# Performance work log

Hardware: AMD Instinct MI355X
Metric: run time of the kernel (lower is better)

## Reference

```python
import jax, jax.numpy as jnp
import numpy as np

B, T, C, H = 4, 2048, 1024, 16
D = C // H  # head dim = 64

def precompute_rope(dim, max_pos):
    # rope_cache[t, i] = (cos(t*theta_i), sin(t*theta_i)), theta_i = 10000^(-2i/dim)
    i = jnp.arange(dim // 2, dtype=jnp.float32)
    theta = 1.0 / (10000.0 ** (2.0 * i / dim))
    t = jnp.arange(max_pos, dtype=jnp.float32)[:, None]
    ang = t * theta[None, :]
    return jnp.stack([jnp.cos(ang), jnp.sin(ang)], axis=-1)  # (max_pos, dim/2, 2)

def apply_rope(x, rope):
    # x: (B, H, T, D); complex multiply rope * x over pairs of channels
    Tq = x.shape[2]
    xr = x.reshape(x.shape[0], x.shape[1], Tq, D // 2, 2)
    a, b = xr[..., 0], xr[..., 1]
    c = rope[:Tq, :, 0]  # (T, D/2)
    s = rope[:Tq, :, 1]
    real = a * c - b * s
    imag = a * s + b * c
    return jnp.stack([real, imag], axis=-1).reshape(x.shape)

def setup_inputs() -> dict:
    key = jax.random.key(0)
    ks = jax.random.split(key, 9)
    scale = 1.0 / np.sqrt(C)
    def w(k):
        return jax.random.uniform(k, (C, C), jnp.float32, -scale, scale)
    def bvec(k):
        return jax.random.uniform(k, (C,), jnp.float32, -scale, scale)
    return {
        "x": jax.random.normal(ks[0], (B, T, C), jnp.float32),
        "Wq": w(ks[1]), "bq": bvec(ks[2]),
        "Wk": w(ks[3]), "bk": bvec(ks[4]),
        "Wv": w(ks[5]), "bv": bvec(ks[6]),
        "Wp": w(ks[7]), "bp": bvec(ks[8]),
        "rope_cache": precompute_rope(D, T),
    }

def reference(x, Wq, bq, Wk, bk, Wv, bv, Wp, bp, rope_cache):
    B_, T_, C_ = x.shape
    def heads(y):
        return y.reshape(B_, T_, H, D).transpose(0, 2, 1, 3)  # (B,H,T,D)
    q = heads(x @ Wq.T + bq)
    k = heads(x @ Wk.T + bk)
    v = heads(x @ Wv.T + bv)
    q = apply_rope(q, rope_cache)
    k = apply_rope(k, rope_cache)
    att = jnp.einsum("bhqd,bhkd->bhqk", q, k) * (1.0 / np.sqrt(D))
    causal = jnp.tril(jnp.ones((T_, T_), dtype=bool))
    att = jnp.where(causal, att, jnp.float32(-1e10))
    att = jax.nn.softmax(att, axis=-1)
    y = jnp.einsum("bhqk,bhkd->bhqd", att, v)
    y = y.transpose(0, 2, 1, 3).reshape(B_, T_, C_)
    return y @ Wp.T + bp
```

## Files before the change

kernel.cpp:

```cpp
#include <hip/hip_runtime.h>

#define DEVINL __device__ __forceinline__

typedef unsigned short u16;
typedef __attribute__((ext_vector_type(4))) short s16x4;
typedef __attribute__((ext_vector_type(8))) short s16x8;
typedef __attribute__((ext_vector_type(4))) float f32x4;

static constexpr int Bb = 4, Tt = 2048, Cc = 1024, Hh = 16, Dd = 64;
static constexpr int Mm = Bb * Tt;
static constexpr int KK = Cc;

DEVINL float bf2f(u16 u) { return __uint_as_float(((unsigned)u) << 16); }
DEVINL u16 f2bf(float f) {
  unsigned b = __float_as_uint(f);
  b += 0x7fff + ((b >> 16) & 1);
  return (u16)(b >> 16);
}
DEVINL unsigned cvtpk(float lo, float hi) {
  unsigned r;
  asm("v_cvt_pk_bf16_f32 %0, %1, %2" : "=v"(r) : "v"(lo), "v"(hi));
  return r;
}

#define GLDS(gsrc, ldst) \
  __builtin_amdgcn_global_load_lds((const __attribute__((address_space(1))) void*)(gsrc), \
                                   (__attribute__((address_space(3))) void*)(ldst), 16, 0, 0)

__global__ void cvt_bf16(const float* __restrict__ src, u16* __restrict__ dst, int n4) {
  int i = blockIdx.x * blockDim.x + threadIdx.x;
  int st = gridDim.x * blockDim.x;
  for (int g = i; g < n4; g += st) {
    float4 v = ((const float4*)src)[g];
    uint2 o;
    o.x = (unsigned)f2bf(v.x) | ((unsigned)f2bf(v.y) << 16);
    o.y = (unsigned)f2bf(v.z) | ((unsigned)f2bf(v.w) << 16);
    ((uint2*)dst)[g] = o;
  }
}

struct Cvt4Args { const float* s[4]; u16* d[4]; };
__global__ void cvt4(Cvt4Args a, int n4) {
  const float* __restrict__ src = a.s[blockIdx.y];
  u16* __restrict__ dst = a.d[blockIdx.y];
  int i = blockIdx.x * blockDim.x + threadIdx.x;
  int st = gridDim.x * blockDim.x;
  for (int g = i; g < n4; g += st) {
    float4 v = ((const float4*)src)[g];
    uint2 o;
    o.x = (unsigned)f2bf(v.x) | ((unsigned)f2bf(v.y) << 16);
    o.y = (unsigned)f2bf(v.z) | ((unsigned)f2bf(v.w) << 16);
    ((uint2*)dst)[g] = o;
  }
}

__global__ void rope_kernel(u16* __restrict__ q, u16* __restrict__ k,
                            const float* __restrict__ cache) {
  const float CS = 0.18033688f;
  const int total = Bb * Hh * Tt * 8;
  int i = blockIdx.x * blockDim.x + threadIdx.x;
  int st = gridDim.x * blockDim.x;
  for (int g = i; g < total; g += st) {
    int off = g * 8;
    int t = (off >> 6) & (Tt - 1);
    int d0 = off & 63;
    const float* cp = cache + t * 64 + d0;
    float4 c0 = *(const float4*)cp;
    float4 c1 = *(const float4*)(cp + 4);
    float cs[8] = {c0.x, c0.y, c0.z, c0.w, c1.x, c1.y, c1.z, c1.w};
    s16x8 qv = *(s16x8*)(q + off);
    s16x8 kv = *(s16x8*)(k + off);
    s16x8 qo, ko;
#pragma unroll
    for (int p = 0; p < 4; ++p) {
      float c = cs[2 * p], s = cs[2 * p + 1];
      float a = bf2f((u16)qv[2 * p]), b = bf2f((u16)qv[2 * p + 1]);
      qo[2 * p] = (short)f2bf((a * c - b * s) * CS);
      qo[2 * p + 1] = (short)f2bf((a * s + b * c) * CS);
      a = bf2f((u16)kv[2 * p]); b = bf2f((u16)kv[2 * p + 1]);
      ko[2 * p] = (short)f2bf(a * c - b * s);
      ko[2 * p + 1] = (short)f2bf(a * s + b * c);
    }
    *(s16x8*)(q + off) = qo;
    *(s16x8*)(k + off) = ko;
  }
}

#define GEMM_PROLOG()                                              \
  const int tid = threadIdx.x, w = tid >> 6, l = tid & 63;         \
  const int lr = l & 15, lg = l >> 4;                              \
  const int m0 = blockIdx.x * 128, n0 = blockIdx.y * 128;          \
  const int wr = w >> 1, wc = w & 1;                               \
  f32x4 zero = {0.f, 0.f, 0.f, 0.f};                               \
  f32x4 acc[4][4];                                                 \
  _Pragma("unroll") for (int i = 0; i < 4; ++i)                    \
      _Pragma("unroll") for (int j = 0; j < 4; ++j) acc[i][j] = zero; \
  const int srow = l >> 3;                                         \
  const int scolsw = ((l & 7) ^ (l >> 3)) * 8;

#define GEMM_KLOOP(Aptr, Wptr)                                                         \
  for (int k0 = 0; k0 < KK; k0 += 64) {                                                \
    _Pragma("unroll") for (int i = 0; i < 4; ++i) {                                    \
      int row = i * 32 + w * 8 + srow;                                                 \
      GLDS(Aptr + (size_t)(m0 + row) * KK + k0 + scolsw, &As[(i * 32 + w * 8) * 64]);  \
      GLDS(Wptr + (size_t)(n0 + row) * KK + k0 + scolsw, &Bs[(i * 32 + w * 8) * 64]);  \
    }                                                                                  \
    __syncthreads();                                                                   \
    _Pragma("unroll") for (int kk = 0; kk < 2; ++kk) {                                 \
      s16x8 af[4], bfr[4];                                                             \
      _Pragma("unroll") for (int i = 0; i < 4; ++i)                                    \
          af[i] = *(const s16x8*)&As[(wr * 64 + i * 16 + lr) * 64 +                    \
                                     ((kk * 32 + lg * 8) ^ ((lr & 7) << 3))];          \
      _Pragma("unroll") for (int j = 0; j < 4; ++j)                                    \
          bfr[j] = *(const s16x8*)&Bs[(wc * 64 + j * 16 + lr) * 64 +                   \
                                      ((kk * 32 + lg * 8) ^ ((lr & 7) << 3))];         \
      _Pragma("unroll") for (int i = 0; i < 4; ++i)                                    \
          _Pragma("unroll") for (int j = 0; j < 4; ++j)                                \
              acc[i][j] =                                                              \
                  __builtin_amdgcn_mfma_f32_16x16x32_bf16(af[i], bfr[j], acc[i][j], 0, 0, 0); \
    }                                                                                  \
    __syncthreads();                                                                   \
  }

__global__ __launch_bounds__(256) void gemm_qk(const u16* __restrict__ A,
                                               const u16* __restrict__ W0,
                                               const u16* __restrict__ W1,
                                               const float* __restrict__ b0,
                                               const float* __restrict__ b1,
                                               u16* __restrict__ O0, u16* __restrict__ O1) {
  __shared__ __align__(16) u16 As[128 * 64];
  __shared__ __align__(16) u16 Bs[128 * 64];
  const int z = blockIdx.z;
  const u16* __restrict__ Wt = z ? W1 : W0;
  const float* __restrict__ bias = z ? b1 : b0;
  u16* __restrict__ O = z ? O1 : O0;
  GEMM_PROLOG()
  GEMM_KLOOP(A, Wt)
#pragma unroll
  for (int j = 0; j < 4; ++j) {
    int ncol = n0 + wc * 64 + j * 16 + lr;
    float bj = bias[ncol];
    int hh = ncol >> 6, dd = ncol & 63;
#pragma unroll
    for (int i = 0; i < 4; ++i) {
#pragma unroll
      for (int r = 0; r < 4; ++r) {
        int mrow = m0 + wr * 64 + i * 16 + lg * 4 + r;
        int bb2 = mrow >> 11, tt2 = mrow & (Tt - 1);
        O[(((size_t)bb2 * Hh + hh) * Tt + tt2) * Dd + dd] = f2bf(acc[i][j][r] + bj);
      }
    }
  }
}

__global__ __launch_bounds__(256) void gemm_v(const u16* __restrict__ A,
                                              const u16* __restrict__ Wt,
                                              const float* __restrict__ bias,
                                              u16* __restrict__ O) {
  __shared__ __align__(16) u16 As[128 * 64];
  __shared__ __align__(16) u16 Bs[128 * 64];
  __shared__ __align__(16) u16 Ts[128 * 64];
  GEMM_PROLOG()
  GEMM_KLOOP(A, Wt)
  const int bb2 = m0 >> 11, tloc = m0 & (Tt - 1);
#pragma unroll
  for (int p = 0; p < 2; ++p) {
    if (p) __syncthreads();
    if (wr == p) {
#pragma unroll
      for (int j = 0; j < 4; ++j) {
        int ncl = wc * 64 + j * 16 + lr;
        float bj = bias[n0 + ncl];
        int xw = (ncl & 3) << 2;
#pragma unroll
        for (int i = 0; i < 4; ++i) {
          s16x4 pk;
#pragma unroll
          for (int r = 0; r < 4; ++r) pk[r] = (short)f2bf(acc[i][j][r] + bj);
          *(s16x4*)&Ts[ncl * 64 + (((i * 4 + lg) ^ xw) << 2)] = pk;
        }
      }
    }
    __syncthreads();
    const int rn = tid >> 3, t8 = tid & 7;
#pragma unroll
    for (int it = 0; it < 4; ++it) {
      int rown = it * 32 + rn;
      int slot = (t8 * 2) ^ ((rown & 3) << 2);
      s16x8 v = *(const s16x8*)&Ts[rown * 64 + slot * 4];
      int ncol = n0 + rown;
      int hh2 = ncol >> 6, dd = ncol & 63;
      *(s16x8*)&O[(((size_t)bb2 * Hh + hh2) * Dd + dd) * Tt + tloc + p * 64 + t8 * 8] = v;
    }
  }
}

__global__ __launch_bounds__(256) void gemm_proj(const u16* __restrict__ A,
                                                 const u16* __restrict__ Wt,
                                                 const float* __restrict__ bias,
                                                 float* __restrict__ O) {
  __shared__ __align__(16) u16 As[128 * 64];
  __shared__ __align__(16) u16 Bs[128 * 64];
  GEMM_PROLOG()
  GEMM_KLOOP(A, Wt)
#pragma unroll
  for (int j = 0; j < 4; ++j) {
    int ncol = n0 + wc * 64 + j * 16 + lr;
    float bj = bias[ncol];
#pragma unroll
    for (int i = 0; i < 4; ++i) {
#pragma unroll
      for (int r = 0; r < 4; ++r) {
        int mrow = m0 + wr * 64 + i * 16 + lg * 4 + r;
        O[(size_t)mrow * Cc + ncol] = acc[i][j][r] + bj;
      }
    }
  }
}

__global__ __launch_bounds__(256, 4) void attn_kernel(const u16* __restrict__ Q,
                                                      const u16* __restrict__ K,
                                                      const u16* __restrict__ VTg,
                                                      u16* __restrict__ Out) {
  __shared__ __align__(16) u16 Ks[2][64 * 64];
  __shared__ __align__(16) u16 VTs[2][64 * 64];
  __shared__ __align__(16) u16 Ps[4 * 16 * 32];
  const int tid = threadIdx.x, w = tid >> 6, l = tid & 63;
  const int lr = l & 15, lg = l >> 4;
  const int n = blockIdx.x + 16 * blockIdx.y;
  const int bh = ((n & 7) << 3) + (n >> 7);
  const int qpair = (n >> 3) & 15;
  const size_t base = (size_t)bh * Tt * Dd;
  const u16* Qp = Q + base;
  const u16* Kp = K + base;
  const u16* Vp = VTg + base;
  const int bb2 = bh >> 4, hh = bh & 15;
  const float NEG = -3.0e9f;
  f32x4 zero = {0.f, 0.f, 0.f, 0.f};
  const int krow_l = l >> 3, kc8sw = ((l & 7) ^ (l >> 3)) * 8;
  const int psw = (lr >> 1) & 3;

  auto process = [&](int qt) {
    const int qb0 = qt * 64;
    const int qrow = qb0 + w * 16 + lr;
    const int qg = qrow;
    s16x8 qf[2];
    qf[0] = *(const s16x8*)(Qp + (size_t)qrow * 64 + lg * 8);
    qf[1] = *(const s16x8*)(Qp + (size_t)qrow * 64 + 32 + lg * 8);
    f32x4 o[4] = {zero, zero, zero, zero};
    float m = -3e38f, lsum = 0.f;
    const int ktiles = qt + 1;
    auto stage = [&](int kt, int buf) {
      const int kk0 = kt * 64;
#pragma unroll
      for (int i = 0; i < 2; ++i) {
        int row = i * 32 + w * 8 + krow_l;
        GLDS(Kp + (size_t)(kk0 + row) * 64 + kc8sw, &Ks[buf][(i * 32 + w * 8) * 64]);
        GLDS(Vp + (size_t)row * Tt + kk0 + kc8sw, &VTs[buf][(i * 32 + w * 8) * 64]);
      }
    };
    stage(0, 0);
    for (int kt = 0; kt < ktiles; ++kt) {
      const int buf = kt & 1;
      if (kt + 1 < ktiles) {
        stage(kt + 1, buf ^ 1);
        asm volatile("s_waitcnt vmcnt(4)" ::: "memory");
      } else {
        asm volatile("s_waitcnt vmcnt(0)" ::: "memory");
      }
      __builtin_amdgcn_s_barrier();
      __builtin_amdgcn_sched_barrier(0);
      float pv[4][4];
      const int diag = (kt == ktiles - 1);
      __builtin_amdgcn_s_setprio(1);
#pragma unroll
      for (int cf = 0; cf < 4; ++cf) {
        f32x4 s = zero;
#pragma unroll
        for (int kf = 0; kf < 2; ++kf) {
          s16x8 kb = *(const s16x8*)&Ks[buf][(cf * 16 + lr) * 64 +
                                            (((kf * 4 + lg) ^ (lr & 7)) << 3)];
          s = __builtin_amdgcn_mfma_f32_16x16x32_bf16(kb, qf[kf], s, 0, 0, 0);
        }
        if (diag) {
          int key0 = kt * 64 + cf * 16 + lg * 4;
#pragma unroll
          for (int r = 0; r < 4; ++r) pv[cf][r] = (key0 + r <= qg) ? s[r] : NEG;
        } else {
#pragma unroll
          for (int r = 0; r < 4; ++r) pv[cf][r] = s[r];
        }
      }
      __builtin_amdgcn_s_setprio(0);
      float t0 = fmaxf(fmaxf(pv[0][0], pv[0][1]), fmaxf(pv[0][2], pv[0][3]));
#pragma unroll
      for (int cf = 1; cf < 4; ++cf) {
        float tc = fmaxf(fmaxf(pv[cf][0], pv[cf][1]), fmaxf(pv[cf][2], pv[cf][3]));
        t0 = fmaxf(t0, tc);
      }
      t0 = fmaxf(t0, __shfl_xor(t0, 16));
      float tm = fmaxf(t0, __shfl_xor(t0, 32));
      int stable = tm <= m + 11.5f;
      if (!__all(stable)) {
        float mn = fmaxf(m, tm);
        float fsc = __builtin_amdgcn_exp2f(m - mn);
        lsum *= fsc;
        m = mn;
#pragma unroll
        for (int jf = 0; jf < 4; ++jf) {
          o[jf][0] *= fsc; o[jf][1] *= fsc; o[jf][2] *= fsc; o[jf][3] *= fsc;
        }
      }
      float psum = 0.f;
#pragma unroll
      for (int cf = 0; cf < 4; ++cf)
#pragma unroll
        for (int r = 0; r < 4; ++r) {
          float p = __builtin_amdgcn_exp2f(pv[cf][r] - m);
          pv[cf][r] = p;
          psum += p;
        }
      psum += __shfl_xor(psum, 16);
      psum += __shfl_xor(psum, 32);
      lsum += psum;
#pragma unroll
      for (int kk = 0; kk < 2; ++kk) {
#pragma unroll
        for (int c = 0; c < 2; ++c) {
          int cf = kk * 2 + c;
          unsigned w0 = cvtpk(pv[cf][0], pv[cf][1]);
          unsigned w1 = cvtpk(pv[cf][2], pv[cf][3]);
          int col0 = c * 16 + lg * 4;
          int idx = w * 512 + lr * 32 + ((((col0 >> 3) ^ psw)) << 3) + (col0 & 7);
          *(unsigned*)&Ps[idx] = w0;
          *(unsigned*)&Ps[idx + 2] = w1;
        }
        s16x8 pa = *(const s16x8*)&Ps[w * 512 + lr * 32 + ((lg ^ psw) << 3)];
        __builtin_amdgcn_s_setprio(1);
#pragma unroll
        for (int jf = 0; jf < 4; ++jf) {
          s16x8 vb = *(const s16x8*)&VTs[buf][(jf * 16 + lr) * 64 +
                                             (((kk * 4 + lg) ^ (lr & 7)) << 3)];
          o[jf] = __builtin_amdgcn_mfma_f32_16x16x32_bf16(vb, pa, o[jf], 0, 0, 0);
        }
        __builtin_amdgcn_s_setprio(0);
      }
      __builtin_amdgcn_sched_barrier(0);
      __builtin_amdgcn_s_barrier();
    }
    float linv = 1.0f / lsum;
    int tq = qb0 + w * 16 + lr;
    u16* orow = Out + ((size_t)(bb2 * Tt + tq)) * Cc + hh * 64 + lg * 4;
#pragma unroll
    for (int jf = 0; jf < 4; ++jf) {
      uint2 pk;
      pk.x = cvtpk(o[jf][0] * linv, o[jf][1] * linv);
      pk.y = cvtpk(o[jf][2] * linv, o[jf][3] * linv);
      *(uint2*)&orow[jf * 16] = pk;
    }
  };

  process(qpair);
  process(31 - qpair);
}

extern "C" void kernel_launch(void* const* d_in, const int* in_sizes, int n_in,
                              void* d_out, int out_size, void* d_ws, size_t ws_size,
                              hipStream_t stream) {
  (void)in_sizes; (void)n_in; (void)out_size; (void)ws_size;
  const float* x = (const float*)d_in[0];
  const float* Wq = (const float*)d_in[1];
  const float* bq = (const float*)d_in[2];
  const float* Wk = (const float*)d_in[3];
  const float* bk = (const float*)d_in[4];
  const float* Wv = (const float*)d_in[5];
  const float* bv = (const float*)d_in[6];
  const float* Wp = (const float*)d_in[7];
  const float* bp = (const float*)d_in[8];
  const float* rope = (const float*)d_in[9];

  char* ws = (char*)d_ws;
  const size_t MB = 1024 * 1024;
  u16* xb  = (u16*)(ws + 0);
  u16* wqb = (u16*)(ws + 16 * MB);
  u16* wkb = (u16*)(ws + 18 * MB);
  u16* wvb = (u16*)(ws + 20 * MB);
  u16* wpb = (u16*)(ws + 22 * MB);
  u16* qb  = (u16*)(ws + 24 * MB);
  u16* kb  = (u16*)(ws + 40 * MB);
  u16* vt  = (u16*)(ws + 56 * MB);
  u16* att = (u16*)(ws + 72 * MB);

  cvt_bf16<<<2048, 256, 0, stream>>>(x, xb, (Mm * Cc) / 4);
  Cvt4Args ca;
  ca.s[0] = Wq; ca.s[1] = Wk; ca.s[2] = Wv; ca.s[3] = Wp;
  ca.d[0] = wqb; ca.d[1] = wkb; ca.d[2] = wvb; ca.d[3] = wpb;
  cvt4<<<dim3(256, 4), 256, 0, stream>>>(ca, (Cc * Cc) / 4);

  gemm_qk<<<dim3(Mm / 128, Cc / 128, 2), 256, 0, stream>>>(xb, wqb, wkb, bq, bk, qb, kb);
  gemm_v<<<dim3(Mm / 128, Cc / 128), 256, 0, stream>>>(xb, wvb, bv, vt);

  rope_kernel<<<2048, 256, 0, stream>>>(qb, kb, rope);

  attn_kernel<<<dim3(16, Bb * Hh), 256, 0, stream>>>(qb, kb, vt, att);

  gemm_proj<<<dim3(Mm / 128, Cc / 128), 256, 0, stream>>>(att, wpb, bp, (float*)d_out);
}
```

Measured before the change: 185.8 us.

## Fuse RoPE into QK GEMM epilogue and co-process paired query tiles in attention

Removes the standalone rope kernel and applies the rotary embedding, plus the softmax scale on Q, inside the QK projection epilogue. Adjacent channel pairs are exchanged with a lane shuffle, which avoids a full read-modify-write pass over Q and K. The attention kernel now handles the low and high query tiles of each block in one shared K/V loop instead of two sequential passes. Each K/V tile is staged once and used by both query tiles, at the cost of holding two sets of accumulators and raising register pressure.

Result: slower. 228.2 us (+22.9%).

```diff
diff --git a/kernel.cpp b/kernel.cpp
--- a/kernel.cpp
+++ b/kernel.cpp
@@ -51,38 +51,6 @@
     o.x = (unsigned)f2bf(v.x) | ((unsigned)f2bf(v.y) << 16);
     o.y = (unsigned)f2bf(v.z) | ((unsigned)f2bf(v.w) << 16);
     ((uint2*)dst)[g] = o;
-  }
-}
-
-__global__ void rope_kernel(u16* __restrict__ q, u16* __restrict__ k,
-                            const float* __restrict__ cache) {
-  const float CS = 0.18033688f;
-  const int total = Bb * Hh * Tt * 8;
-  int i = blockIdx.x * blockDim.x + threadIdx.x;
-  int st = gridDim.x * blockDim.x;
-  for (int g = i; g < total; g += st) {
-    int off = g * 8;
-    int t = (off >> 6) & (Tt - 1);
-    int d0 = off & 63;
-    const float* cp = cache + t * 64 + d0;
-    float4 c0 = *(const float4*)cp;
-    float4 c1 = *(const float4*)(cp + 4);
-    float cs[8] = {c0.x, c0.y, c0.z, c0.w, c1.x, c1.y, c1.z, c1.w};
-    s16x8 qv = *(s16x8*)(q + off);
-    s16x8 kv = *(s16x8*)(k + off);
-    s16x8 qo, ko;
-#pragma unroll
-    for (int p = 0; p < 4; ++p) {
-      float c = cs[2 * p], s = cs[2 * p + 1];
-      float a = bf2f((u16)qv[2 * p]), b = bf2f((u16)qv[2 * p + 1]);
-      qo[2 * p] = (short)f2bf((a * c - b * s) * CS);
-      qo[2 * p + 1] = (short)f2bf((a * s + b * c) * CS);
-      a = bf2f((u16)kv[2 * p]); b = bf2f((u16)kv[2 * p + 1]);
-      ko[2 * p] = (short)f2bf(a * c - b * s);
-      ko[2 * p + 1] = (short)f2bf(a * s + b * c);
-    }
-    *(s16x8*)(q + off) = qo;
-    *(s16x8*)(k + off) = ko;
   }
 }
 
@@ -127,6 +95,7 @@
                                                const u16* __restrict__ W1,
                                                const float* __restrict__ b0,
                                                const float* __restrict__ b1,
+                                               const float* __restrict__ rope,
                                                u16* __restrict__ O0, u16* __restrict__ O1) {
   __shared__ __align__(16) u16 As[128 * 64];
   __shared__ __align__(16) u16 Bs[128 * 64];
@@ -134,6 +103,7 @@
   const u16* __restrict__ Wt = z ? W1 : W0;
   const float* __restrict__ bias = z ? b1 : b0;
   u16* __restrict__ O = z ? O1 : O0;
+  const float scl = z ? 1.0f : 0.18033688f;
   GEMM_PROLOG()
   GEMM_KLOOP(A, Wt)
 #pragma unroll
@@ -141,13 +111,19 @@
     int ncol = n0 + wc * 64 + j * 16 + lr;
     float bj = bias[ncol];
     int hh = ncol >> 6, dd = ncol & 63;
+    const float sign = (dd & 1) ? 1.0f : -1.0f;
+    const float* csp = rope + (dd >> 1) * 2;
 #pragma unroll
     for (int i = 0; i < 4; ++i) {
 #pragma unroll
       for (int r = 0; r < 4; ++r) {
         int mrow = m0 + wr * 64 + i * 16 + lg * 4 + r;
         int bb2 = mrow >> 11, tt2 = mrow & (Tt - 1);
-        O[(((size_t)bb2 * Hh + hh) * Tt + tt2) * Dd + dd] = f2bf(acc[i][j][r] + bj);
+        float v = acc[i][j][r] + bj;
+        float part = __shfl_xor(v, 1);
+        float2 cs = *(const float2*)(csp + tt2 * 64);
+        float outv = (v * cs.x + sign * part * cs.y) * scl;
+        O[(((size_t)bb2 * Hh + hh) * Tt + tt2) * Dd + dd] = f2bf(outv);
       }
     }
   }
@@ -229,7 +205,8 @@
   const int lr = l & 15, lg = l >> 4;
   const int n = blockIdx.x + 16 * blockIdx.y;
   const int bh = ((n & 7) << 3) + (n >> 7);
-  const int qpair = (n >> 3) & 15;
+  const int qt = (n >> 3) & 15;
+  const int qtH = 31 - qt;
   const size_t base = (size_t)bh * Tt * Dd;
   const u16* Qp = Q + base;
   const u16* Kp = K + base;
@@ -240,128 +217,144 @@
   const int krow_l = l >> 3, kc8sw = ((l & 7) ^ (l >> 3)) * 8;
   const int psw = (lr >> 1) & 3;
 
-  auto process = [&](int qt) {
-    const int qb0 = qt * 64;
-    const int qrow = qb0 + w * 16 + lr;
-    const int qg = qrow;
-    s16x8 qf[2];
-    qf[0] = *(const s16x8*)(Qp + (size_t)qrow * 64 + lg * 8);
-    qf[1] = *(const s16x8*)(Qp + (size_t)qrow * 64 + 32 + lg * 8);
-    f32x4 o[4] = {zero, zero, zero, zero};
-    float m = -3e38f, lsum = 0.f;
-    const int ktiles = qt + 1;
-    auto stage = [&](int kt, int buf) {
-      const int kk0 = kt * 64;
-#pragma unroll
-      for (int i = 0; i < 2; ++i) {
-        int row = i * 32 + w * 8 + krow_l;
-        GLDS(Kp + (size_t)(kk0 + row) * 64 + kc8sw, &Ks[buf][(i * 32 + w * 8) * 64]);
-        GLDS(Vp + (size_t)row * Tt + kk0 + kc8sw, &VTs[buf][(i * 32 + w * 8) * 64]);
-      }
-    };
-    stage(0, 0);
-    for (int kt = 0; kt < ktiles; ++kt) {
-      const int buf = kt & 1;
-      if (kt + 1 < ktiles) {
-        stage(kt + 1, buf ^ 1);
-        asm volatile("s_waitcnt vmcnt(4)" ::: "memory");
+  const int qgL = qt * 64 + w * 16 + lr, qgH = qtH * 64 + w * 16 + lr;
+  s16x8 qfL[2], qfH[2];
+  qfL[0] = *(const s16x8*)(Qp + (size_t)qgL * 64 + lg * 8);
+  qfL[1] = *(const s16x8*)(Qp + (size_t)qgL * 64 + 32 + lg * 8);
+  qfH[0] = *(const s16x8*)(Qp + (size_t)qgH * 64 + lg * 8);
+  qfH[1] = *(const s16x8*)(Qp + (size_t)qgH * 64 + 32 + lg * 8);
+  f32x4 oL[4] = {zero, zero, zero, zero};
+  f32x4 oH[4] = {zero, zero, zero, zero};
+  float mL = -3e38f, lsL = 0.f, mH = -3e38f, lsH = 0.f;
+
+  auto stage = [&](int kt, int buf) {
+    const int kk0 = kt * 64;
+#pragma unroll
+    for (int i = 0; i < 2; ++i) {
+      int row = i * 32 + w * 8 + krow_l;
+      GLDS(Kp + (size_t)(kk0 + row) * 64 + kc8sw, &Ks[buf][(i * 32 + w * 8) * 64]);
+      GLDS(Vp + (size_t)row * Tt + kk0 + kc8sw, &VTs[buf][(i * 32 + w * 8) * 64]);
+    }
+  };
+
+  auto tile = [&](int kt, int buf, f32x4 (&o)[4], const s16x8 (&qf)[2],
+                  float& m, float& lsum, int qg, bool diag) {
+    float pv[4][4];
+    __builtin_amdgcn_s_setprio(1);
+#pragma unroll
+    for (int cf = 0; cf < 4; ++cf) {
+      f32x4 s = zero;
+#pragma unroll
+      for (int kf = 0; kf < 2; ++kf) {
+        s16x8 kb = *(const s16x8*)&Ks[buf][(cf * 16 + lr) * 64 +
+                                          (((kf * 4 + lg) ^ (lr & 7)) << 3)];
+        s = __builtin_amdgcn_mfma_f32_16x16x32_bf16(kb, qf[kf], s, 0, 0, 0);
+      }
+      if (diag) {
+        int key0 = kt * 64 + cf * 16 + lg * 4;
+#pragma unroll
+        for (int r = 0; r < 4; ++r) pv[cf][r] = (key0 + r <= qg) ? s[r] : NEG;
       } else {
-        asm volatile("s_waitcnt vmcnt(0)" ::: "memory");
-      }
-      __builtin_amdgcn_s_barrier();
-      __builtin_amdgcn_sched_barrier(0);
-      float pv[4][4];
-      const int diag = (kt == ktiles - 1);
+#pragma unroll
+        for (int r = 0; r < 4; ++r) pv[cf][r] = s[r];
+      }
+    }
+    __builtin_amdgcn_s_setprio(0);
+    float t0 = fmaxf(fmaxf(pv[0][0], pv[0][1]), fmaxf(pv[0][2], pv[0][3]));
+#pragma unroll
+    for (int cf = 1; cf < 4; ++cf) {
+      float tc = fmaxf(fmaxf(pv[cf][0], pv[cf][1]), fmaxf(pv[cf][2], pv[cf][3]));
+      t0 = fmaxf(t0, tc);
+    }
+    t0 = fmaxf(t0, __shfl_xor(t0, 16));
+    float tm = fmaxf(t0, __shfl_xor(t0, 32));
+    int stable = tm <= m + 11.5f;
+    if (!__all(stable)) {
+      float mn = fmaxf(m, tm);
+      float fsc = __builtin_amdgcn_exp2f(m - mn);
+      lsum *= fsc;
+      m = mn;
+#pragma unroll
+      for (int jf = 0; jf < 4; ++jf) {
+        o[jf][0] *= fsc; o[jf][1] *= fsc; o[jf][2] *= fsc; o[jf][3] *= fsc;
+      }
+    }
+    float psum = 0.f;
+#pragma unroll
+    for (int cf = 0; cf < 4; ++cf)
+#pragma unroll
+      for (int r = 0; r < 4; ++r) {
+        float p = __builtin_amdgcn_exp2f(pv[cf][r] - m);
+        pv[cf][r] = p;
+        psum += p;
+      }
+    psum += __shfl_xor(psum, 16);
+    psum += __shfl_xor(psum, 32);
+    lsum += psum;
+#pragma unroll
+    for (int kk = 0; kk < 2; ++kk) {
+#pragma unroll
+      for (int c = 0; c < 2; ++c) {
+        int cf = kk * 2 + c;
+        unsigned w0 = cvtpk(pv[cf][0], pv[cf][1]);
+        unsigned w1 = cvtpk(pv[cf][2], pv[cf][3]);
+        int col0 = c * 16 + lg * 4;
+        int idx = w * 512 + lr * 32 + ((((col0 >> 3) ^ psw)) << 3) + (col0 & 7);
+        *(unsigned*)&Ps[idx] = w0;
+        *(unsigned*)&Ps[idx + 2] = w1;
+      }
+      s16x8 pa = *(const s16x8*)&Ps[w * 512 + lr * 32 + ((lg ^ psw) << 3)];
       __builtin_amdgcn_s_setprio(1);
 #pragma unroll
-      for (int cf = 0; cf < 4; ++cf) {
-        f32x4 s = zero;
-#pragma unroll
-        for (int kf = 0; kf < 2; ++kf) {
-          s16x8 kb = *(const s16x8*)&Ks[buf][(cf * 16 + lr) * 64 +
-                                            (((kf * 4 + lg) ^ (lr & 7)) << 3)];
-          s = __builtin_amdgcn_mfma_f32_16x16x32_bf16(kb, qf[kf], s, 0, 0, 0);
-        }
-        if (diag) {
-          int key0 = kt * 64 + cf * 16 + lg * 4;
-#pragma unroll
-          for (int r = 0; r < 4; ++r) pv[cf][r] = (key0 + r <= qg) ? s[r] : NEG;
-        } else {
-#pragma unroll
-          for (int r = 0; r < 4; ++r) pv[cf][r] = s[r];
-        }
+      for (int jf = 0; jf < 4; ++jf) {
+        s16x8 vb = *(const s16x8*)&VTs[buf][(jf * 16 + lr) * 64 +
+                                           (((kk * 4 + lg) ^ (lr & 7)) << 3)];
+        o[jf] = __builtin_amdgcn_mfma_f32_16x16x32_bf16(vb, pa, o[jf], 0, 0, 0);
       }
       __builtin_amdgcn_s_setprio(0);
-      float t0 = fmaxf(fmaxf(pv[0][0], pv[0][1]), fmaxf(pv[0][2], pv[0][3]));
-#pragma unroll
-      for (int cf = 1; cf < 4; ++cf) {
-        float tc = fmaxf(fmaxf(pv[cf][0], pv[cf][1]), fmaxf(pv[cf][2], pv[cf][3]));
-        t0 = fmaxf(t0, tc);
-      }
-      t0 = fmaxf(t0, __shfl_xor(t0, 16));
-      float tm = fmaxf(t0, __shfl_xor(t0, 32));
-      int stable = tm <= m + 11.5f;
-      if (!__all(stable)) {
-        float mn = fmaxf(m, tm);
-        float fsc = __builtin_amdgcn_exp2f(m - mn);
-        lsum *= fsc;
-        m = mn;
-#pragma unroll
-        for (int jf = 0; jf < 4; ++jf) {
-          o[jf][0] *= fsc; o[jf][1] *= fsc; o[jf][2] *= fsc; o[jf][3] *= fsc;
-        }
-      }
-      float psum = 0.f;
-#pragma unroll
-      for (int cf = 0; cf < 4; ++cf)
-#pragma unroll
-        for (int r = 0; r < 4; ++r) {
-          float p = __builtin_amdgcn_exp2f(pv[cf][r] - m);
-          pv[cf][r] = p;
-          psum += p;
-        }
-      psum += __shfl_xor(psum, 16);
-      psum += __shfl_xor(psum, 32);
-      lsum += psum;
-#pragma unroll
-      for (int kk = 0; kk < 2; ++kk) {
-#pragma unroll
-        for (int c = 0; c < 2; ++c) {
-          int cf = kk * 2 + c;
-          unsigned w0 = cvtpk(pv[cf][0], pv[cf][1]);
-          unsigned w1 = cvtpk(pv[cf][2], pv[cf][3]);
-          int col0 = c * 16 + lg * 4;
-          int idx = w * 512 + lr * 32 + ((((col0 >> 3) ^ psw)) << 3) + (col0 & 7);
-          *(unsigned*)&Ps[idx] = w0;
-          *(unsigned*)&Ps[idx + 2] = w1;
-        }
-        s16x8 pa = *(const s16x8*)&Ps[w * 512 + lr * 32 + ((lg ^ psw) << 3)];
-        __builtin_amdgcn_s_setprio(1);
-#pragma unroll
-        for (int jf = 0; jf < 4; ++jf) {
-          s16x8 vb = *(const s16x8*)&VTs[buf][(jf * 16 + lr) * 64 +
-                                             (((kk * 4 + lg) ^ (lr & 7)) << 3)];
-          o[jf] = __builtin_amdgcn_mfma_f32_16x16x32_bf16(vb, pa, o[jf], 0, 0, 0);
-        }
-        __builtin_amdgcn_s_setprio(0);
-      }
-      __builtin_amdgcn_sched_barrier(0);
-      __builtin_amdgcn_s_barrier();
-    }
-    float linv = 1.0f / lsum;
-    int tq = qb0 + w * 16 + lr;
-    u16* orow = Out + ((size_t)(bb2 * Tt + tq)) * Cc + hh * 64 + lg * 4;
+    }
+  };
+
+  const int htiles = qtH + 1;
+  stage(0, 0);
+  for (int kt = 0; kt < htiles; ++kt) {
+    const int buf = kt & 1;
+    if (kt + 1 < htiles) {
+      stage(kt + 1, buf ^ 1);
+      asm volatile("s_waitcnt vmcnt(4)" ::: "memory");
+    } else {
+      asm volatile("s_waitcnt vmcnt(0)" ::: "memory");
+    }
+    __builtin_amdgcn_s_barrier();
+    __builtin_amdgcn_sched_barrier(0);
+    tile(kt, buf, oH, qfH, mH, lsH, qgH, kt == qtH);
+    if (kt <= qt)
+      tile(kt, buf, oL, qfL, mL, lsL, qgL, kt == qt);
+    __builtin_amdgcn_sched_barrier(0);
+    __builtin_amdgcn_s_barrier();
+  }
+  {
+    float linv = 1.0f / lsL;
+    u16* orow = Out + ((size_t)(bb2 * Tt + qgL)) * Cc + hh * 64 + lg * 4;
 #pragma unroll
     for (int jf = 0; jf < 4; ++jf) {
       uint2 pk;
-      pk.x = cvtpk(o[jf][0] * linv, o[jf][1] * linv);
-      pk.y = cvtpk(o[jf][2] * linv, o[jf][3] * linv);
+      pk.x = cvtpk(oL[jf][0] * linv, oL[jf][1] * linv);
+      pk.y = cvtpk(oL[jf][2] * linv, oL[jf][3] * linv);
       *(uint2*)&orow[jf * 16] = pk;
     }
-  };
-
-  process(qpair);
-  process(31 - qpair);
+  }
+  {
+    float linv = 1.0f / lsH;
+    u16* orow = Out + ((size_t)(bb2 * Tt + qgH)) * Cc + hh * 64 + lg * 4;
+#pragma unroll
+    for (int jf = 0; jf < 4; ++jf) {
+      uint2 pk;
+      pk.x = cvtpk(oH[jf][0] * linv, oH[jf][1] * linv);
+      pk.y = cvtpk(oH[jf][2] * linv, oH[jf][3] * linv);
+      *(uint2*)&orow[jf * 16] = pk;
+    }
+  }
 }
 
 extern "C" void kernel_launch(void* const* d_in, const int* in_sizes, int n_in,
@@ -397,11 +390,9 @@
   ca.d[0] = wqb; ca.d[1] = wkb; ca.d[2] = wvb; ca.d[3] = wpb;
   cvt4<<<dim3(256, 4), 256, 0, stream>>>(ca, (Cc * Cc) / 4);
 
-  gemm_qk<<<dim3(Mm / 128, Cc / 128, 2), 256, 0, stream>>>(xb, wqb, wkb, bq, bk, qb, kb);
+  gemm_qk<<<dim3(Mm / 128, Cc / 128, 2), 256, 0, stream>>>(xb, wqb, wkb, bq, bk, rope, qb, kb);
   gemm_v<<<dim3(Mm / 128, Cc / 128), 256, 0, stream>>>(xb, wvb, bv, vt);
 
-  rope_kernel<<<2048, 256, 0, stream>>>(qb, kb, rope);
-
   attn_kernel<<<dim3(16, Bb * Hh), 256, 0, stream>>>(qb, kb, vt, att);
 
   gemm_proj<<<dim3(Mm / 128, Cc / 128), 256, 0, stream>>>(att, wpb, bp, (float*)d_out);
```

## Double-buffer GEMM LDS staging and fuse RoPE into QK projection epilogue

Applied to the files above, without the earlier changes.

The GEMM k-loop now double-buffers the shared-memory tiles, so the next K slice is loaded while the current one feeds the MFMAs. It waits with a partial vmcnt and raw barriers instead of full syncs. RoPE and the Q scaling move into the QK GEMM epilogue, with a lane-xor shuffle pairing adjacent channels. This drops the separate rope kernel and its extra read/write pass over Q and K. LDS per block doubles, which may lower occupancy, and the epilogue gains per-element cache loads.

Result: faster. 174.7 us (-6.0%).

```diff
diff --git a/kernel.cpp b/kernel.cpp
--- a/kernel.cpp
+++ b/kernel.cpp
@@ -54,38 +54,6 @@
   }
 }
 
-__global__ void rope_kernel(u16* __restrict__ q, u16* __restrict__ k,
-                            const float* __restrict__ cache) {
-  const float CS = 0.18033688f;
-  const int total = Bb * Hh * Tt * 8;
-  int i = blockIdx.x * blockDim.x + threadIdx.x;
-  int st = gridDim.x * blockDim.x;
-  for (int g = i; g < total; g += st) {
-    int off = g * 8;
-    int t = (off >> 6) & (Tt - 1);
-    int d0 = off & 63;
-    const float* cp = cache + t * 64 + d0;
-    float4 c0 = *(const float4*)cp;
-    float4 c1 = *(const float4*)(cp + 4);
-    float cs[8] = {c0.x, c0.y, c0.z, c0.w, c1.x, c1.y, c1.z, c1.w};
-    s16x8 qv = *(s16x8*)(q + off);
-    s16x8 kv = *(s16x8*)(k + off);
-    s16x8 qo, ko;
-#pragma unroll
-    for (int p = 0; p < 4; ++p) {
-      float c = cs[2 * p], s = cs[2 * p + 1];
-      float a = bf2f((u16)qv[2 * p]), b = bf2f((u16)qv[2 * p + 1]);
-      qo[2 * p] = (short)f2bf((a * c - b * s) * CS);
-      qo[2 * p + 1] = (short)f2bf((a * s + b * c) * CS);
-      a = bf2f((u16)kv[2 * p]); b = bf2f((u16)kv[2 * p + 1]);
-      ko[2 * p] = (short)f2bf(a * c - b * s);
-      ko[2 * p + 1] = (short)f2bf(a * s + b * c);
-    }
-    *(s16x8*)(q + off) = qo;
-    *(s16x8*)(k + off) = ko;
-  }
-}
-
 #define GEMM_PROLOG()                                              \
   const int tid = threadIdx.x, w = tid >> 6, l = tid & 63;         \
   const int lr = l & 15, lg = l >> 4;                              \
@@ -98,28 +66,40 @@
   const int srow = l >> 3;                                         \
   const int scolsw = ((l & 7) ^ (l >> 3)) * 8;
 
-#define GEMM_KLOOP(Aptr, Wptr)                                                         \
-  for (int k0 = 0; k0 < KK; k0 += 64) {                                                \
-    _Pragma("unroll") for (int i = 0; i < 4; ++i) {                                    \
-      int row = i * 32 + w * 8 + srow;                                                 \
-      GLDS(Aptr + (size_t)(m0 + row) * KK + k0 + scolsw, &As[(i * 32 + w * 8) * 64]);  \
-      GLDS(Wptr + (size_t)(n0 + row) * KK + k0 + scolsw, &Bs[(i * 32 + w * 8) * 64]);  \
-    }                                                                                  \
-    __syncthreads();                                                                   \
-    _Pragma("unroll") for (int kk = 0; kk < 2; ++kk) {                                 \
-      s16x8 af[4], bfr[4];                                                             \
-      _Pragma("unroll") for (int i = 0; i < 4; ++i)                                    \
-          af[i] = *(const s16x8*)&As[(wr * 64 + i * 16 + lr) * 64 +                    \
-                                     ((kk * 32 + lg * 8) ^ ((lr & 7) << 3))];          \
-      _Pragma("unroll") for (int j = 0; j < 4; ++j)                                    \
-          bfr[j] = *(const s16x8*)&Bs[(wc * 64 + j * 16 + lr) * 64 +                   \
-                                      ((kk * 32 + lg * 8) ^ ((lr & 7) << 3))];         \
-      _Pragma("unroll") for (int i = 0; i < 4; ++i)                                    \
-          _Pragma("unroll") for (int j = 0; j < 4; ++j)                                \
-              acc[i][j] =                                                              \
+#define GEMM_STAGE(Aptr, Wptr, k0, buf)                                                  \
+  _Pragma("unroll") for (int i = 0; i < 4; ++i) {                                        \
+    int row = i * 32 + w * 8 + srow;                                                     \
+    GLDS(Aptr + (size_t)(m0 + row) * KK + (k0) + scolsw, &As[buf][(i * 32 + w * 8) * 64]); \
+    GLDS(Wptr + (size_t)(n0 + row) * KK + (k0) + scolsw, &Bs[buf][(i * 32 + w * 8) * 64]); \
+  }
+
+#define GEMM_KLOOP_DB(Aptr, Wptr)                                                        \
+  GEMM_STAGE(Aptr, Wptr, 0, 0)                                                           \
+  for (int k0 = 0; k0 < KK; k0 += 64) {                                                  \
+    const int buf = (k0 >> 6) & 1;                                                       \
+    if (k0 + 64 < KK) {                                                                  \
+      GEMM_STAGE(Aptr, Wptr, k0 + 64, buf ^ 1)                                           \
+      asm volatile("s_waitcnt vmcnt(8)" ::: "memory");            \
+    } else {                                                                             \
+      asm volatile("s_waitcnt vmcnt(0)" ::: "memory");                                   \
+    }                                                                                    \
+    __builtin_amdgcn_s_barrier();                                                        \
+    __builtin_amdgcn_sched_barrier(0);                                                   \
+    _Pragma("unroll") for (int kk = 0; kk < 2; ++kk) {                                   \
+      s16x8 af[4], bfr[4];                                                               \
+      _Pragma("unroll") for (int i = 0; i < 4; ++i)                                      \
+          af[i] = *(const s16x8*)&As[buf][(wr * 64 + i * 16 + lr) * 64 +                 \
+                                         ((kk * 32 + lg * 8) ^ ((lr & 7) << 3))];        \
+      _Pragma("unroll") for (int j = 0; j < 4; ++j)                                      \
+          bfr[j] = *(const s16x8*)&Bs[buf][(wc * 64 + j * 16 + lr) * 64 +                \
+                                          ((kk * 32 + lg * 8) ^ ((lr & 7) << 3))];       \
+      _Pragma("unroll") for (int i = 0; i < 4; ++i)                                      \
+          _Pragma("unroll") for (int j = 0; j < 4; ++j)                                  \
+              acc[i][j] =                                                                \
                   __builtin_amdgcn_mfma_f32_16x16x32_bf16(af[i], bfr[j], acc[i][j], 0, 0, 0); \
-    }                                                                                  \
-    __syncthreads();                                                                   \
+    }                                                                                    \
+    __builtin_amdgcn_sched_barrier(0);                                                   \
+    __builtin_amdgcn_s_barrier();       \
   }
 
 __global__ __launch_bounds__(256) void gemm_qk(const u16* __restrict__ A,
@@ -127,27 +107,35 @@
                                                const u16* __restrict__ W1,
                                                const float* __restrict__ b0,
                                                const float* __restrict__ b1,
+                                               const float* __restrict__ rope,
                                                u16* __restrict__ O0, u16* __restrict__ O1) {
-  __shared__ __align__(16) u16 As[128 * 64];
-  __shared__ __align__(16) u16 Bs[128 * 64];
+  __shared__ __align__(16) u16 As[2][128 * 64];
+  __shared__ __align__(16) u16 Bs[2][128 * 64];
   const int z = blockIdx.z;
   const u16* __restrict__ Wt = z ? W1 : W0;
   const float* __restrict__ bias = z ? b1 : b0;
   u16* __restrict__ O = z ? O1 : O0;
+  const float scl = z ? 1.0f : 0.18033688f;
   GEMM_PROLOG()
-  GEMM_KLOOP(A, Wt)
+  GEMM_KLOOP_DB(A, Wt)
 #pragma unroll
   for (int j = 0; j < 4; ++j) {
     int ncol = n0 + wc * 64 + j * 16 + lr;
     float bj = bias[ncol];
     int hh = ncol >> 6, dd = ncol & 63;
+    const float sign = (dd & 1) ? 1.0f : -1.0f;
+    const float* csp = rope + (dd >> 1) * 2;
 #pragma unroll
     for (int i = 0; i < 4; ++i) {
 #pragma unroll
       for (int r = 0; r < 4; ++r) {
         int mrow = m0 + wr * 64 + i * 16 + lg * 4 + r;
         int bb2 = mrow >> 11, tt2 = mrow & (Tt - 1);
-        O[(((size_t)bb2 * Hh + hh) * Tt + tt2) * Dd + dd] = f2bf(acc[i][j][r] + bj);
+        float v = acc[i][j][r] + bj;
+        float part = __shfl_xor(v, 1);
+        float2 cs = *(const float2*)(csp + tt2 * 64);
+        float outv = (v * cs.x + sign * part * cs.y) * scl;
+        O[(((size_t)bb2 * Hh + hh) * Tt + tt2) * Dd + dd] = f2bf(outv);
       }
     }
   }
@@ -157,11 +145,11 @@
                                               const u16* __restrict__ Wt,
                                               const float* __restrict__ bias,
                                               u16* __restrict__ O) {
-  __shared__ __align__(16) u16 As[128 * 64];
-  __shared__ __align__(16) u16 Bs[128 * 64];
+  __shared__ __align__(16) u16 As[2][128 * 64];
+  __shared__ __align__(16) u16 Bs[2][128 * 64];
   __shared__ __align__(16) u16 Ts[128 * 64];
   GEMM_PROLOG()
-  GEMM_KLOOP(A, Wt)
+  GEMM_KLOOP_DB(A, Wt)
   const int bb2 = m0 >> 11, tloc = m0 & (Tt - 1);
 #pragma unroll
   for (int p = 0; p < 2; ++p) {
@@ -199,10 +187,10 @@
                                                  const u16* __restrict__ Wt,
                                                  const float* __restrict__ bias,
                                                  float* __restrict__ O) {
-  __shared__ __align__(16) u16 As[128 * 64];
-  __shared__ __align__(16) u16 Bs[128 * 64];
+  __shared__ __align__(16) u16 As[2][128 * 64];
+  __shared__ __align__(16) u16 Bs[2][128 * 64];
   GEMM_PROLOG()
-  GEMM_KLOOP(A, Wt)
+  GEMM_KLOOP_DB(A, Wt)
 #pragma unroll
   for (int j = 0; j < 4; ++j) {
     int ncol = n0 + wc * 64 + j * 16 + lr;
@@ -397,11 +385,9 @@
   ca.d[0] = wqb; ca.d[1] = wkb; ca.d[2] = wvb; ca.d[3] = wpb;
   cvt4<<<dim3(256, 4), 256, 0, stream>>>(ca, (Cc * Cc) / 4);
 
-  gemm_qk<<<dim3(Mm / 128, Cc / 128, 2), 256, 0, stream>>>(xb, wqb, wkb, bq, bk, qb, kb);
+  gemm_qk<<<dim3(Mm / 128, Cc / 128, 2), 256, 0, stream>>>(xb, wqb, wkb, bq, bk, rope, qb, kb);
   gemm_v<<<dim3(Mm / 128, Cc / 128), 256, 0, stream>>>(xb, wvb, bv, vt);
 
-  rope_kernel<<<2048, 256, 0, stream>>>(qb, kb, rope);
-
   attn_kernel<<<dim3(16, Bb * Hh), 256, 0, stream>>>(qb, kb, vt, att);
 
   gemm_proj<<<dim3(Mm / 128, Cc / 128), 256, 0, stream>>>(att, wpb, bp, (float*)d_out);
```
